# Optimization experiments

Hardware: AMD Instinct MI355X
Metric: run time of the kernel (lower is better)

The kernel has to match this reference:

```python
import jax, jax.numpy as jnp
import numpy as np

B = 2
SP = (480, 360, 32)   # spatial_shape (z, y, x)
GS = (8, 8, 8)        # query_gs_ratio
EP = (40, 15, 16)     # embed_params (pool compress ratio)
H = 8
N = 120000
D = 256
OUT = 20


def _dims(rat):
    return tuple((s + r - 1) // r for s, r in zip(SP, rat))


def sine_pe(coords, d_pos):
    # coords: [M,3] float voxel coords in original grid units; normalized sine PE
    nf = d_pos // 6
    sp = jnp.asarray(SP, jnp.float32)
    cn = coords / sp * (2.0 * jnp.pi)                      # normalize=True
    t = 10000.0 ** (jnp.arange(nf, dtype=jnp.float32) / nf)
    ang = cn[:, :, None] / t                               # [M,3,nf]
    pe = jnp.concatenate([jnp.sin(ang), jnp.cos(ang)], -1).reshape(coords.shape[0], -1)
    return jnp.pad(pe, ((0, 0), (0, d_pos - 6 * nf)))


def setup_inputs() -> dict:
    key = jax.random.key(0)
    ks = jax.random.split(key, 24)
    idx_b = jax.random.randint(ks[0], (N, 1), 0, B)
    idx_z = jax.random.randint(ks[1], (N, 1), 0, SP[0])
    idx_y = jax.random.randint(ks[2], (N, 1), 0, SP[1])
    idx_x = jax.random.randint(ks[3], (N, 1), 0, SP[2])
    indices = jnp.concatenate([idx_b, idx_z, idx_y, idx_x], axis=1).astype(jnp.int32)
    s = D ** -0.5
    p = lambda k, sh: jax.random.normal(k, sh, jnp.float32) * s
    return {
        'features': jax.random.normal(ks[4], (N, D), jnp.float32),
        'W_pool': p(ks[5], (D, D)), 'b_pool': jnp.zeros((D,), jnp.float32),
        'W_emb': p(ks[6], (D, D)), 'b_emb': jnp.zeros((D,), jnp.float32),
        'Wq': p(ks[7], (D, D)), 'bq': jnp.zeros((D,), jnp.float32),
        'Wk': p(ks[8], (D, D)), 'bk': jnp.zeros((D,), jnp.float32),
        'Wv': p(ks[9], (D, D)), 'bv': jnp.zeros((D,), jnp.float32),
        'Wo': p(ks[10], (D, D)), 'bo': jnp.zeros((D,), jnp.float32),
        'ln_g': jnp.ones((D,), jnp.float32), 'ln_b': jnp.zeros((D,), jnp.float32),
        'W_seg': p(ks[11], (D, OUT)), 'b_seg': jnp.zeros((OUT,), jnp.float32),
        'indices': indices,
        'batch_size': B,
    }


def reference(features, W_pool, b_pool, W_emb, b_emb, Wq, bq, Wk, bk, Wv, bv,
              Wo, bo, ln_g, ln_b, W_seg, b_seg, indices, batch_size):
    Zd, Yd, Xd = _dims(GS)
    Gq = Zd * Yd * Xd
    Sq = batch_size * Gq
    Ze, Ye, Xe = _dims(EP)
    Gk = Ze * Ye * Xe
    Sk = batch_size * Gk
    n = features.shape[0]

    # --- query pool branch: linear -> voxel-grid scatter_max ---
    pf = features @ W_pool + b_pool                                    # [N,D]
    dq = indices[:, 1:] // jnp.asarray(GS, jnp.int32)
    seg_q = ((indices[:, 0] * Zd + dq[:, 0]) * Yd + dq[:, 1]) * Xd + dq[:, 2]
    pool_max = jax.ops.segment_max(pf, seg_q, num_segments=Sq)
    cnt_q = jax.ops.segment_sum(jnp.ones((n,), jnp.float32), seg_q, num_segments=Sq)
    mq = cnt_q > 0
    pool_max = jnp.where(mq[:, None], pool_max, 0.0)
    cell = jnp.arange(Sq)
    rem = cell % Gq
    pool_c = jnp.stack([(rem // (Yd * Xd)) * GS[0],
                        ((rem // Xd) % Yd) * GS[1],
                        (rem % Xd) * GS[2]], -1).astype(jnp.float32)   # [Sq,3]

    # --- embedding branch ('pool'): linear -> coarse scatter_max + per-channel argmax coords ---
    ef = features @ W_emb + b_emb                                      # [N,D]
    de = indices[:, 1:] // jnp.asarray(EP, jnp.int32)
    seg_k = ((indices[:, 0] * Ze + de[:, 0]) * Ye + de[:, 1]) * Xe + de[:, 2]
    emb_max = jax.ops.segment_max(ef, seg_k, num_segments=Sk)
    cnt_k = jax.ops.segment_sum(jnp.ones((n,), jnp.float32), seg_k, num_segments=Sk)
    mk = cnt_k > 0
    emb_max = jnp.where(mk[:, None], emb_max, 0.0)
    winner = ef == jnp.where(mk[:, None], emb_max, -jnp.inf)[seg_k]
    idx = jax.ops.segment_max(jnp.where(winner, jnp.arange(n)[:, None], -1), seg_k, num_segments=Sk)
    idx_c = jnp.clip(idx, 0, n - 1)                                    # [Sk,D]
    ec = de.astype(jnp.float32)                                        # [N,3] downsampled coords
    emb_c = ec[idx_c].mean(axis=1) * jnp.asarray(EP, jnp.float32)      # [Sk,3]

    # --- position encoding (pointwise sine PE; per-batch loop in torch is pointwise-equivalent) ---
    pool_max = pool_max + sine_pe(pool_c, D)
    emb_max = emb_max + sine_pe(emb_c, D)

    # --- multi-head cross-attention (Q=pool, K/V=embedding), per-batch via dense grid reshape ---
    q_in = pool_max.reshape(batch_size, Gq, D)
    kv_in = emb_max.reshape(batch_size, Gk, D)
    dh = D // H
    q = (q_in @ Wq + bq).reshape(batch_size, Gq, H, dh)
    k = (kv_in @ Wk + bk).reshape(batch_size, Gk, H, dh)
    v = (kv_in @ Wv + bv).reshape(batch_size, Gk, H, dh)
    scores = jnp.einsum('bqhd,bkhd->bhqk', q, k) / jnp.float32(dh) ** 0.5
    kmask = mk.reshape(batch_size, Gk)
    scores = jnp.where(kmask[:, None, None, :], scores, -1e9)
    attn = jax.nn.softmax(scores, axis=-1)
    o = jnp.einsum('bhqk,bkhd->bqhd', attn, v).reshape(batch_size, Gq, D) @ Wo + bo
    h = q_in + o                                                       # residual + LayerNorm sublayer
    mu = h.mean(-1, keepdims=True)
    var = h.var(-1, keepdims=True)
    h = (h - mu) * jax.lax.rsqrt(var + 1e-5) * ln_g + ln_b
    feats_mhca = h.reshape(Sq, D)

    # --- gather back to voxels via pool_inv, residual, seg head (center-tap of SubMConv3d) ---
    vox = features + feats_mhca[seg_q]
    logits = vox @ W_seg + b_seg
    return logits
```

## Files before the change

kernel.cpp:

```cpp
#include <hip/hip_runtime.h>
#include <math.h>

#define N_PTS 120000
#define D 256
#define BATCH 2
#define NH 8
#define DH 32
#define OUTC 20

#define Zd 60
#define Yd 45
#define Xd 4
#define Gq 10800
#define Sq 21600

#define Ze 12
#define Ye 24
#define Xe 2
#define Gk 576
#define Sk 1152

typedef __bf16 bf16_t;
typedef __attribute__((ext_vector_type(8))) __bf16 bf16x8;
typedef __attribute__((ext_vector_type(4))) __bf16 bf16x4;
typedef __attribute__((ext_vector_type(4))) float f32x4;

__global__ __launch_bounds__(256) void k_prep(
    const float* __restrict__ Wp, const float* __restrict__ We,
    const float* __restrict__ Wq, const float* __restrict__ Wk,
    const float* __restrict__ Wv, const float* __restrict__ Wo,
    const float* __restrict__ bp, const float* __restrict__ be,
    const float* __restrict__ bk, const float* __restrict__ bv,
    bf16_t* __restrict__ Wpe, bf16_t* __restrict__ Wqt,
    bf16_t* __restrict__ Wkv, bf16_t* __restrict__ Wot,
    float* __restrict__ bpe, float* __restrict__ bkv)
{
    int n = blockIdx.x, k = threadIdx.x;
    if (n < 512) {
        const float* S = (n < 256) ? Wp : We;
        int nn = n & 255;
        Wpe[n * 256 + k] = (bf16_t)S[k * 256 + nn];
    } else if (n < 768) {
        int nn = n - 512;
        Wqt[nn * 256 + k] = (bf16_t)Wq[k * 256 + nn];
    } else if (n < 1280) {
        int m2 = n - 768;
        const float* S = (m2 < 256) ? Wk : Wv;
        int nn = m2 & 255;
        Wkv[m2 * 256 + k] = (bf16_t)S[k * 256 + nn];
    } else if (n < 1536) {
        int nn = n - 1280;
        Wot[nn * 256 + k] = (bf16_t)Wo[k * 256 + nn];
    } else {
        bpe[k] = bp[k]; bpe[256 + k] = be[k];
        bkv[k] = bk[k]; bkv[256 + k] = bv[k];
    }
}

__global__ __launch_bounds__(256) void k_count(
    const int* __restrict__ indices, int* __restrict__ cnt_q, int* __restrict__ cnt_k,
    int* __restrict__ segq, int* __restrict__ segk)
{
    int i = blockIdx.x * 256 + threadIdx.x;
    if (i >= N_PTS) return;
    const int* id = indices + (size_t)i * 4;
    int b = id[0], z = id[1], y = id[2], x = id[3];
    int sq = ((b * Zd + (z >> 3)) * Yd + (y >> 3)) * Xd + (x >> 3);
    int sk = ((b * Ze + (z / 40)) * Ye + (y / 15)) * Xe + (x >> 4);
    segq[i] = sq; segk[i] = sk;
    atomicAdd(&cnt_q[sq], 1);
    atomicAdd(&cnt_k[sk], 1);
}

__global__ __launch_bounds__(1024) void k_scan(
    const int* __restrict__ cnt, int n, int* __restrict__ offs, int* __restrict__ cursor)
{
    __shared__ int wbase[17];
    __shared__ int carry_s;
    const int t = threadIdx.x, lane = t & 63, w = t >> 6;
    if (t == 0) carry_s = 0;
    __syncthreads();
    for (int base = 0; base < n; base += 1024) {
        int v = (base + t < n) ? cnt[base + t] : 0;
        int incl = v;
        #pragma unroll
        for (int off = 1; off < 64; off <<= 1) {
            int u = __shfl_up(incl, off);
            if (lane >= off) incl += u;
        }
        if (lane == 63) wbase[w + 1] = incl;
        __syncthreads();
        if (t == 0) {
            int s = 0;
            wbase[0] = 0;
            #pragma unroll
            for (int i = 1; i <= 16; ++i) { s += wbase[i]; wbase[i] = s; }
        }
        __syncthreads();
        int excl = incl - v + wbase[w] + carry_s;
        if (base + t < n) { offs[base + t] = excl; cursor[base + t] = excl; }
        __syncthreads();
        if (t == 0) carry_s += wbase[16];
        __syncthreads();
    }
}

__global__ __launch_bounds__(256) void k_place(
    const int* __restrict__ segq, const int* __restrict__ segk,
    int* __restrict__ cur_q, int* __restrict__ cur_k,
    int* __restrict__ ids_q, int* __restrict__ ids_k)
{
    int i = blockIdx.x * 256 + threadIdx.x;
    if (i >= N_PTS) return;
    ids_q[atomicAdd(&cur_q[segq[i]], 1)] = i;
    ids_k[atomicAdd(&cur_k[segk[i]], 1)] = i;
}

__global__ __launch_bounds__(512, 2) void k_gemm(
    const float* __restrict__ A, int M,
    const bf16_t* __restrict__ Wt, const float* __restrict__ bias,
    int mode, float* __restrict__ outp, int ldo)
{
    __shared__ __align__(16) bf16_t Abuf[128][72];
    __shared__ __align__(16) bf16_t Bbuf[256][72];

    const int t = threadIdx.x;
    const int wave = t >> 6, lane = t & 63;
    const int wr = wave >> 2, wc = wave & 3;
    const int lrow = lane & 15, quad = lane >> 4;
    const int row0 = blockIdx.y * 128;
    const int ntile = blockIdx.x;

    f32x4 acc[4][4];
    #pragma unroll
    for (int mi = 0; mi < 4; ++mi)
        #pragma unroll
        for (int ni = 0; ni < 4; ++ni)
            acc[mi][ni] = (f32x4){0.f, 0.f, 0.f, 0.f};

    for (int k0 = 0; k0 < 256; k0 += 64) {
        #pragma unroll
        for (int i = 0; i < 4; ++i) {
            int c = i * 512 + t;
            int r = c >> 4, c4 = c & 15;
            float4 v = make_float4(0.f, 0.f, 0.f, 0.f);
            if (row0 + r < M)
                v = *(const float4*)(A + (size_t)(row0 + r) * 256 + k0 + c4 * 4);
            bf16x4 bv4;
            bv4[0] = (bf16_t)v.x; bv4[1] = (bf16_t)v.y;
            bv4[2] = (bf16_t)v.z; bv4[3] = (bf16_t)v.w;
            *(bf16x4*)&Abuf[r][c4 * 4] = bv4;
        }
        #pragma unroll
        for (int i = 0; i < 4; ++i) {
            int c = i * 512 + t;
            int r = c >> 3, c8 = c & 7;
            uint4 w = *(const uint4*)(Wt + ((size_t)(ntile * 256 + r)) * 256 + k0 + c8 * 8);
            *(uint4*)&Bbuf[r][c8 * 8] = w;
        }
        __syncthreads();

        #pragma unroll
        for (int kk = 0; kk < 64; kk += 32) {
            bf16x8 Af[4], Bf[4];
            #pragma unroll
            for (int mi = 0; mi < 4; ++mi)
                Af[mi] = *(const bf16x8*)&Abuf[wr * 64 + mi * 16 + lrow][kk + quad * 8];
            #pragma unroll
            for (int ni = 0; ni < 4; ++ni)
                Bf[ni] = *(const bf16x8*)&Bbuf[wc * 64 + ni * 16 + lrow][kk + quad * 8];
            #pragma unroll
            for (int mi = 0; mi < 4; ++mi)
                #pragma unroll
                for (int ni = 0; ni < 4; ++ni)
                    acc[mi][ni] = __builtin_amdgcn_mfma_f32_16x16x32_bf16(
                        Af[mi], Bf[ni], acc[mi][ni], 0, 0, 0);
        }
        __syncthreads();
    }

    const int colb = ntile * 256 + wc * 64;
    float biasv[4];
    #pragma unroll
    for (int ni = 0; ni < 4; ++ni) biasv[ni] = bias[colb + ni * 16 + lrow];

    if (mode == 0) {
        #pragma unroll
        for (int mi = 0; mi < 4; ++mi) {
            int lr = wr * 64 + mi * 16 + quad * 4;
            #pragma unroll
            for (int reg = 0; reg < 4; ++reg) {
                int grow = row0 + lr + reg;
                if (grow >= M) continue;
                #pragma unroll
                for (int ni = 0; ni < 4; ++ni) {
                    int col = colb + ni * 16 + lrow;
                    outp[(size_t)grow * ldo + col] = acc[mi][ni][reg] + biasv[ni];
                }
            }
        }
    } else {
        bf16_t* outb = (bf16_t*)outp;
        #pragma unroll
        for (int mi = 0; mi < 4; ++mi) {
            int lr = wr * 64 + mi * 16 + quad * 4;
            #pragma unroll
            for (int reg = 0; reg < 4; ++reg) {
                int grow = row0 + lr + reg;
                if (grow >= M) continue;
                #pragma unroll
                for (int ni = 0; ni < 4; ++ni) {
                    int col = colb + ni * 16 + lrow;
                    outb[(size_t)grow * ldo + col] = (bf16_t)(acc[mi][ni][reg] + biasv[ni]);
                }
            }
        }
    }
}

__device__ inline float pe_val(int j, float cz, float cy, float cx) {
    if (j >= 252) return 0.f;
    int dim = j / 84;
    int f = j % 84;
    int fi = (f >= 42) ? (f - 42) : f;
    float c  = (dim == 0) ? cz : ((dim == 1) ? cy : cx);
    float sp = (dim == 0) ? 480.f : ((dim == 1) ? 360.f : 32.f);
    float cn = c / sp * 6.28318530717958647692f;
    float tt = expf((float)fi * (9.210340371976184f / 42.f));
    float ang = cn / tt;
    return (f >= 42) ? cosf(ang) : sinf(ang);
}

__global__ __launch_bounds__(256) void k_pool_q(
    const bf16_t* __restrict__ pfb, const int* __restrict__ ids,
    const int* __restrict__ offs, const int* __restrict__ cnt,
    float* __restrict__ out)
{
    const int t = threadIdx.x, lane = t & 63, w = t >> 6;
    const int s = blockIdx.x * 4 + w;
    if (s >= Sq) return;
    const int count = cnt[s], start = offs[s];
    float mx[4] = {-3.0e38f, -3.0e38f, -3.0e38f, -3.0e38f};
    for (int r = 0; r < count; ++r) {
        int i = ids[start + r];
        bf16x4 v = *(const bf16x4*)(pfb + (size_t)i * 256 + lane * 4);
        #pragma unroll
        for (int j = 0; j < 4; ++j) mx[j] = fmaxf(mx[j], (float)v[j]);
    }
    int rem = s % Gq;
    float cz = (float)((rem / (Yd * Xd)) * 8);
    float cy = (float)(((rem / Xd) % Yd) * 8);
    float cx = (float)((rem % Xd) * 8);
    #pragma unroll
    for (int j = 0; j < 4; ++j) {
        float v = (count > 0) ? mx[j] : 0.f;
        out[(size_t)s * 256 + lane * 4 + j] = v + pe_val(lane * 4 + j, cz, cy, cx);
    }
}

__global__ __launch_bounds__(512) void k_pool_k(
    const bf16_t* __restrict__ efb, const int* __restrict__ ids,
    const int* __restrict__ offs, const int* __restrict__ cnt,
    float* __restrict__ out, int* __restrict__ kmask)
{
    __shared__ float red[8][256];
    const int t = threadIdx.x, lane = t & 63, w = t >> 6;
    const int s = blockIdx.x;
    const int count = cnt[s], start = offs[s];
    float mx[4] = {-3.0e38f, -3.0e38f, -3.0e38f, -3.0e38f};
    for (int r = w; r < count; r += 8) {
        int i = ids[start + r];
        bf16x4 v = *(const bf16x4*)(efb + (size_t)i * 256 + lane * 4);
        #pragma unroll
        for (int j = 0; j < 4; ++j) mx[j] = fmaxf(mx[j], (float)v[j]);
    }
    #pragma unroll
    for (int j = 0; j < 4; ++j) red[w][lane * 4 + j] = mx[j];
    __syncthreads();
    if (t < 256) {
        float m = red[0][t];
        #pragma unroll
        for (int i = 1; i < 8; ++i) m = fmaxf(m, red[i][t]);
        if (count == 0) m = 0.f;
        int rem = s % Gk;
        float cz = (float)((rem / (Ye * Xe)) * 40);
        float cy = (float)(((rem / Xe) % Ye) * 15);
        float cx = (float)((rem % Xe) * 16);
        out[(size_t)s * 256 + t] = m + pe_val(t, cz, cy, cx);
        if (t == 0) kmask[s] = (count > 0) ? 1 : 0;
    }
}

__global__ __launch_bounds__(256) void k_attn_mfma(
    const bf16_t* __restrict__ Q, const bf16_t* __restrict__ KV,
    const int* __restrict__ kmask, float* __restrict__ O)
{
    __shared__ __align__(16) bf16_t Qs[64][40];
    __shared__ __align__(16) bf16_t Ks[192][40];
    __shared__ __align__(16) bf16_t Vts[32][200];
    __shared__ __align__(16) bf16_t Ps[4][16][200];
    __shared__ float mskf[192];

    const int bh = blockIdx.y;
    const int b = bh >> 3, h = bh & 7;
    const int t = threadIdx.x, wave = t >> 6, lane = t & 63;
    const int lrow = lane & 15, quad = lane >> 4;
    const int q0 = blockIdx.x * 64;

    {
        int r = t >> 2, part = t & 3;
        int qi = q0 + r;
        uint4 val = make_uint4(0u, 0u, 0u, 0u);
        if (qi < Gq)
            val = *(const uint4*)(Q + ((size_t)(b * Gq + qi)) * 256 + h * 32 + part * 8);
        *(uint4*)&Qs[r][part * 8] = val;
    }
    __syncthreads();

    const bf16x8 Aq = *(const bf16x8*)&Qs[wave * 16 + lrow][quad * 8];

    f32x4 oacc[2];
    oacc[0] = (f32x4){0.f, 0.f, 0.f, 0.f};
    oacc[1] = (f32x4){0.f, 0.f, 0.f, 0.f};
    float m_run[4], l_run[4];
    #pragma unroll
    for (int r = 0; r < 4; ++r) { m_run[r] = -3.0e38f; l_run[r] = 0.f; }

    for (int c0 = 0; c0 < Gk; c0 += 192) {
        __syncthreads();
        #pragma unroll
        for (int i = 0; i < 3; ++i) {
            int idx = i * 256 + t;
            int kk = idx >> 2, part = idx & 3;
            uint4 val = *(const uint4*)(KV + ((size_t)(b * Gk + c0 + kk)) * 512 + h * 32 + part * 8);
            *(uint4*)&Ks[kk][part * 8] = val;
        }
        #pragma unroll
        for (int i = 0; i < 3; ++i) {
            int idx = i * 256 + t;
            int kk = idx >> 2, part = idx & 3;
            bf16x8 v = *(const bf16x8*)(KV + ((size_t)(b * Gk + c0 + kk)) * 512 + 256 + h * 32 + part * 8);
            #pragma unroll
            for (int j = 0; j < 8; ++j)
                Vts[part * 8 + j][kk] = v[j];
        }
        if (t < 192) mskf[t] = kmask[b * Gk + c0 + t] ? 0.f : -1.0e9f;
        __syncthreads();

        float sreg[12][4];
        #pragma unroll
        for (int nt = 0; nt < 12; ++nt) {
            bf16x8 Bk = *(const bf16x8*)&Ks[nt * 16 + lrow][quad * 8];
            f32x4 sacc = __builtin_amdgcn_mfma_f32_16x16x32_bf16(
                Aq, Bk, (f32x4){0.f, 0.f, 0.f, 0.f}, 0, 0, 0);
            float pen = mskf[nt * 16 + lrow];
            #pragma unroll
            for (int r = 0; r < 4; ++r)
                sreg[nt][r] = sacc[r] * 0.17677669529663688f + pen;
        }

        float alpha[4];
        #pragma unroll
        for (int r = 0; r < 4; ++r) {
            float mx = sreg[0][r];
            #pragma unroll
            for (int nt = 1; nt < 12; ++nt) mx = fmaxf(mx, sreg[nt][r]);
            #pragma unroll
            for (int off = 1; off < 16; off <<= 1)
                mx = fmaxf(mx, __shfl_xor(mx, off));
            float mnew = fmaxf(m_run[r], mx);
            alpha[r] = __expf(m_run[r] - mnew);
            m_run[r] = mnew;
            l_run[r] *= alpha[r];
        }
        #pragma unroll
        for (int n2 = 0; n2 < 2; ++n2)
            #pragma unroll
            for (int r = 0; r < 4; ++r) oacc[n2][r] *= alpha[r];

        float psum[4] = {0.f, 0.f, 0.f, 0.f};
        #pragma unroll
        for (int nt = 0; nt < 12; ++nt) {
            #pragma unroll
            for (int r = 0; r < 4; ++r) {
                float p = __expf(sreg[nt][r] - m_run[r]);
                psum[r] += p;
                Ps[wave][quad * 4 + r][nt * 16 + lrow] = (bf16_t)p;
            }
        }
        #pragma unroll
        for (int r = 0; r < 4; ++r) {
            float s = psum[r];
            #pragma unroll
            for (int off = 1; off < 16; off <<= 1) s += __shfl_xor(s, off);
            l_run[r] += s;
        }

        #pragma unroll
        for (int ks = 0; ks < 6; ++ks) {
            bf16x8 Ap = *(const bf16x8*)&Ps[wave][lrow][ks * 32 + quad * 8];
            #pragma unroll
            for (int n2 = 0; n2 < 2; ++n2) {
                bf16x8 Bv = *(const bf16x8*)&Vts[n2 * 16 + lrow][ks * 32 + quad * 8];
                oacc[n2] = __builtin_amdgcn_mfma_f32_16x16x32_bf16(
                    Ap, Bv, oacc[n2], 0, 0, 0);
            }
        }
    }

    #pragma unroll
    for (int r = 0; r < 4; ++r) {
        int qi = q0 + wave * 16 + quad * 4 + r;
        if (qi >= Gq) continue;
        float inv = (l_run[r] > 0.f) ? (1.f / l_run[r]) : 0.f;
        #pragma unroll
        for (int n2 = 0; n2 < 2; ++n2)
            O[((size_t)(b * Gq + qi)) * 256 + h * 32 + n2 * 16 + lrow] = oacc[n2][r] * inv;
    }
}

__global__ __launch_bounds__(256) void k_ln(
    const float* __restrict__ oproj, const float* __restrict__ resid,
    const float* __restrict__ g, const float* __restrict__ bta,
    float* __restrict__ out)
{
    const int s = blockIdx.x, t = threadIdx.x;
    float h = resid[(size_t)s * D + t] + oproj[(size_t)s * D + t];

    float s1 = h, s2 = h * h;
    for (int o = 32; o > 0; o >>= 1) {
        s1 += __shfl_down(s1, o);
        s2 += __shfl_down(s2, o);
    }
    __shared__ float r1[4], r2[4];
    __shared__ float mu_s, rstd_s;
    int w = t >> 6;
    if ((t & 63) == 0) { r1[w] = s1; r2[w] = s2; }
    __syncthreads();
    if (t == 0) {
        float a = r1[0] + r1[1] + r1[2] + r1[3];
        float bsum = r2[0] + r2[1] + r2[2] + r2[3];
        float mu = a * (1.f / 256.f);
        float var = bsum * (1.f / 256.f) - mu * mu;
        mu_s = mu;
        rstd_s = rsqrtf(var + 1e-5f);
    }
    __syncthreads();
    out[(size_t)s * D + t] = (h - mu_s) * rstd_s * g[t] + bta[t];
}

#define PTS 16
__global__ __launch_bounds__(320) void k_logits(
    const float* __restrict__ feat, const float* __restrict__ mhca,
    const int* __restrict__ indices, const float* __restrict__ Wseg,
    const float* __restrict__ bseg, float* __restrict__ out)
{
    __shared__ float vox[PTS][D + 1];
    __shared__ float Wl[D * OUTC];
    __shared__ int sq[PTS];
    const int t = threadIdx.x;
    const int p0 = blockIdx.x * PTS;

    if (t < PTS) {
        const int* id = indices + (size_t)(p0 + t) * 4;
        sq[t] = ((id[0] * Zd + (id[1] >> 3)) * Yd + (id[2] >> 3)) * Xd + (id[3] >> 3);
    }
    for (int idx = t; idx < D * OUTC; idx += 320) Wl[idx] = Wseg[idx];
    __syncthreads();
    for (int idx = t; idx < PTS * D; idx += 320) {
        int r = idx / D, k = idx % D;
        vox[r][k] = feat[(size_t)(p0 + r) * D + k] + mhca[(size_t)sq[r] * D + k];
    }
    __syncthreads();

    const int r = t / OUTC, o = t % OUTC;
    float acc = bseg[o];
    #pragma unroll 4
    for (int k = 0; k < D; ++k) acc += vox[r][k] * Wl[k * OUTC + o];
    out[(size_t)(p0 + r) * OUTC + o] = acc;
}

extern "C" void kernel_launch(void* const* d_in, const int* in_sizes, int n_in,
                              void* d_out, int out_size, void* d_ws, size_t ws_size,
                              hipStream_t stream) {
    const float* features = (const float*)d_in[0];
    const float* W_pool = (const float*)d_in[1];
    const float* b_pool = (const float*)d_in[2];
    const float* W_emb  = (const float*)d_in[3];
    const float* b_emb  = (const float*)d_in[4];
    const float* Wq = (const float*)d_in[5];
    const float* bq = (const float*)d_in[6];
    const float* Wk = (const float*)d_in[7];
    const float* bk = (const float*)d_in[8];
    const float* Wv = (const float*)d_in[9];
    const float* bv = (const float*)d_in[10];
    const float* Wo = (const float*)d_in[11];
    const float* bo = (const float*)d_in[12];
    const float* ln_g = (const float*)d_in[13];
    const float* ln_b = (const float*)d_in[14];
    const float* W_seg = (const float*)d_in[15];
    const float* b_seg = (const float*)d_in[16];
    const int* indices = (const int*)d_in[17];
    float* out = (float*)d_out;

    float* ws = (float*)d_ws;
    const size_t SQD = (size_t)Sq * D;
    const size_t SKD = (size_t)Sk * D;
    const size_t PFB_FL = (size_t)N_PTS * D / 2;

    size_t oP   = 0;
    size_t oPF  = oP + PFB_FL;
    size_t oEF  = oPF + SQD;
    size_t oWpe = oEF + SKD;
    size_t oWqt = oWpe + 65536;
    size_t oWkv = oWqt + 32768;
    size_t oWot = oWkv + 65536;
    size_t obpe = oWot + 32768;
    size_t obkv = obpe + 512;
    size_t oCnt = obkv + 512;
    size_t oOffq = oCnt + 21600 + 1152;
    size_t oCurq = oOffq + 21600;
    size_t oOffk = oCurq + 21600;
    size_t oCurk = oOffk + 1152;
    size_t oSegq = oCurk + 1152;
    size_t oSegk = oSegq + N_PTS;
    size_t oIdsq = oSegk + N_PTS;
    size_t oIdsk = oIdsq + N_PTS;
    size_t oKm   = oIdsk + N_PTS;

    bf16_t* pfb = (bf16_t*)(ws + oP);
    float* pool_feat = ws + oPF;
    float* emb_feat  = ws + oEF;
    bf16_t* Wpe = (bf16_t*)(ws + oWpe);
    bf16_t* Wqt = (bf16_t*)(ws + oWqt);
    bf16_t* Wkv = (bf16_t*)(ws + oWkv);
    bf16_t* Wot = (bf16_t*)(ws + oWot);
    float* bpe = ws + obpe;
    float* bkv = ws + obkv;
    int* cnt_q = (int*)(ws + oCnt);
    int* cnt_k = cnt_q + 21600;
    int* offs_q = (int*)(ws + oOffq);
    int* cur_q  = (int*)(ws + oCurq);
    int* offs_k = (int*)(ws + oOffk);
    int* cur_k  = (int*)(ws + oCurk);
    int* segq = (int*)(ws + oSegq);
    int* segk = (int*)(ws + oSegk);
    int* ids_q = (int*)(ws + oIdsq);
    int* ids_k = (int*)(ws + oIdsk);
    int* kmask = (int*)(ws + oKm);

    bf16_t* Qb  = (bf16_t*)(ws + oP);
    bf16_t* KVb = (bf16_t*)(ws + oP + 2764800);
    float* attnO = ws + oP + 3059712;
    float* oproj = ws + oP + 8589312;
    float* mhca  = ws + oP + 3059712;

    hipMemsetAsync(cnt_q, 0, (21600 + 1152) * sizeof(int), stream);

    k_prep<<<1537, 256, 0, stream>>>(W_pool, W_emb, Wq, Wk, Wv, Wo,
                                     b_pool, b_emb, bk, bv,
                                     Wpe, Wqt, Wkv, Wot, bpe, bkv);

    k_count<<<(N_PTS + 255) / 256, 256, 0, stream>>>(indices, cnt_q, cnt_k, segq, segk);
    k_scan<<<1, 1024, 0, stream>>>(cnt_q, 21600, offs_q, cur_q);
    k_scan<<<1, 1024, 0, stream>>>(cnt_k, 1152, offs_k, cur_k);
    k_place<<<(N_PTS + 255) / 256, 256, 0, stream>>>(segq, segk, cur_q, cur_k, ids_q, ids_k);

    {
        dim3 g(1, (N_PTS + 127) / 128);
        k_gemm<<<g, 512, 0, stream>>>(features, N_PTS, Wpe + 256 * 256, bpe + 256, 2,
                                      (float*)pfb, 256);
    }
    k_pool_k<<<Sk, 512, 0, stream>>>(pfb, ids_k, offs_k, cnt_k, emb_feat, kmask);

    {
        dim3 g(1, (N_PTS + 127) / 128);
        k_gemm<<<g, 512, 0, stream>>>(features, N_PTS, Wpe, bpe, 2,
                                      (float*)pfb, 256);
    }
    k_pool_q<<<(Sq + 3) / 4, 256, 0, stream>>>(pfb, ids_q, offs_q, cnt_q, pool_feat);

    {
        dim3 g(1, (Sq + 127) / 128);
        k_gemm<<<g, 512, 0, stream>>>(pool_feat, Sq, Wqt, bq, 2, (float*)Qb, 256);
    }
    {
        dim3 g(2, (Sk + 127) / 128);
        k_gemm<<<g, 512, 0, stream>>>(emb_feat, Sk, Wkv, bkv, 2, (float*)KVb, 512);
    }

    {
        dim3 ag((Gq + 63) / 64, BATCH * NH);
        k_attn_mfma<<<ag, 256, 0, stream>>>(Qb, KVb, kmask, attnO);
    }

    {
        dim3 g(1, (Sq + 127) / 128);
        k_gemm<<<g, 512, 0, stream>>>(attnO, Sq, Wot, bo, 0, oproj, 256);
    }

    k_ln<<<Sq, 256, 0, stream>>>(oproj, pool_feat, ln_g, ln_b, mhca);

    k_logits<<<N_PTS / PTS, 320, 0, stream>>>(
        features, mhca, indices, W_seg, b_seg, out);
}
```

Measured before the change: 708.9 us.

## Rewrite segmentation head logits as bf16 MFMA GEMM with padded weights

Replaces the scalar FMA logits kernel, which processed 16 points per block and reloaded the full seg weight into LDS each time, with a 128-row-tile bf16 MFMA kernel. The W_seg weights are transposed and zero-padded to 32 outputs in the prep kernel. The voxel plus mhca sum is converted to bf16 in LDS before the matrix multiply. This aims to cut per-block weight reload and scalar compute cost, at the price of bf16 rounding on the final projection and wasted work on the padded output columns.

```diff
diff --git a/kernel.cpp b/kernel.cpp
--- a/kernel.cpp
+++ b/kernel.cpp
@@ -31,9 +31,12 @@
     const float* __restrict__ Wv, const float* __restrict__ Wo,
     const float* __restrict__ bp, const float* __restrict__ be,
     const float* __restrict__ bk, const float* __restrict__ bv,
+    const float* __restrict__ Wseg, const float* __restrict__ bseg,
     bf16_t* __restrict__ Wpe, bf16_t* __restrict__ Wqt,
     bf16_t* __restrict__ Wkv, bf16_t* __restrict__ Wot,
-    float* __restrict__ bpe, float* __restrict__ bkv)
+    bf16_t* __restrict__ Wsegt,
+    float* __restrict__ bpe, float* __restrict__ bkv,
+    float* __restrict__ bsegp)
 {
     int n = blockIdx.x, k = threadIdx.x;
     if (n < 512) {
@@ -51,9 +54,13 @@
     } else if (n < 1536) {
         int nn = n - 1280;
         Wot[nn * 256 + k] = (bf16_t)Wo[k * 256 + nn];
-    } else {
+    } else if (n == 1536) {
         bpe[k] = bp[k]; bpe[256 + k] = be[k];
         bkv[k] = bk[k]; bkv[256 + k] = bv[k];
+        if (k < 32) bsegp[k] = (k < OUTC) ? bseg[k] : 0.f;
+    } else {
+        int n2 = n - 1537;
+        Wsegt[n2 * 256 + k] = (n2 < OUTC) ? (bf16_t)Wseg[k * OUTC + n2] : (bf16_t)0.f;
     }
 }
 
@@ -449,35 +456,82 @@
     out[(size_t)s * D + t] = (h - mu_s) * rstd_s * g[t] + bta[t];
 }
 
-#define PTS 16
-__global__ __launch_bounds__(320) void k_logits(
+__global__ __launch_bounds__(512, 2) void k_logits_mfma(
     const float* __restrict__ feat, const float* __restrict__ mhca,
-    const int* __restrict__ indices, const float* __restrict__ Wseg,
-    const float* __restrict__ bseg, float* __restrict__ out)
-{
-    __shared__ float vox[PTS][D + 1];
-    __shared__ float Wl[D * OUTC];
-    __shared__ int sq[PTS];
+    const int* __restrict__ indices, const bf16_t* __restrict__ Wsegt,
+    const float* __restrict__ bsegp, float* __restrict__ out)
+{
+    __shared__ __align__(16) bf16_t Abuf[128][72];
+    __shared__ __align__(16) bf16_t Bbuf[32][72];
+    __shared__ int sq_s[128];
+
     const int t = threadIdx.x;
-    const int p0 = blockIdx.x * PTS;
-
-    if (t < PTS) {
-        const int* id = indices + (size_t)(p0 + t) * 4;
-        sq[t] = ((id[0] * Zd + (id[1] >> 3)) * Yd + (id[2] >> 3)) * Xd + (id[3] >> 3);
-    }
-    for (int idx = t; idx < D * OUTC; idx += 320) Wl[idx] = Wseg[idx];
+    const int wave = t >> 6, lane = t & 63;
+    const int lrow = lane & 15, quad = lane >> 4;
+    const int row0 = blockIdx.x * 128;
+
+    if (t < 128) {
+        int row = row0 + t;
+        if (row < N_PTS) {
+            const int* id = indices + (size_t)row * 4;
+            sq_s[t] = ((id[0] * Zd + (id[1] >> 3)) * Yd + (id[2] >> 3)) * Xd + (id[3] >> 3);
+        } else sq_s[t] = 0;
+    }
     __syncthreads();
-    for (int idx = t; idx < PTS * D; idx += 320) {
-        int r = idx / D, k = idx % D;
-        vox[r][k] = feat[(size_t)(p0 + r) * D + k] + mhca[(size_t)sq[r] * D + k];
-    }
-    __syncthreads();
-
-    const int r = t / OUTC, o = t % OUTC;
-    float acc = bseg[o];
-    #pragma unroll 4
-    for (int k = 0; k < D; ++k) acc += vox[r][k] * Wl[k * OUTC + o];
-    out[(size_t)(p0 + r) * OUTC + o] = acc;
+
+    f32x4 acc[2];
+    acc[0] = (f32x4){0.f, 0.f, 0.f, 0.f};
+    acc[1] = (f32x4){0.f, 0.f, 0.f, 0.f};
+
+    for (int k0 = 0; k0 < 256; k0 += 64) {
+        #pragma unroll
+        for (int i = 0; i < 4; ++i) {
+            int c = i * 512 + t;
+            int r = c >> 4, c4 = c & 15;
+            float4 v = make_float4(0.f, 0.f, 0.f, 0.f);
+            int grow = row0 + r;
+            if (grow < N_PTS) {
+                v = *(const float4*)(feat + (size_t)grow * 256 + k0 + c4 * 4);
+                float4 m = *(const float4*)(mhca + (size_t)sq_s[r] * 256 + k0 + c4 * 4);
+                v.x += m.x; v.y += m.y; v.z += m.z; v.w += m.w;
+            }
+            bf16x4 bv4;
+            bv4[0] = (bf16_t)v.x; bv4[1] = (bf16_t)v.y;
+            bv4[2] = (bf16_t)v.z; bv4[3] = (bf16_t)v.w;
+            *(bf16x4*)&Abuf[r][c4 * 4] = bv4;
+        }
+        if (t < 256) {
+            int r = t >> 3, c8 = t & 7;
+            uint4 w = *(const uint4*)(Wsegt + (size_t)r * 256 + k0 + c8 * 8);
+            *(uint4*)&Bbuf[r][c8 * 8] = w;
+        }
+        __syncthreads();
+
+        #pragma unroll
+        for (int kk = 0; kk < 64; kk += 32) {
+            bf16x8 Af = *(const bf16x8*)&Abuf[wave * 16 + lrow][kk + quad * 8];
+            #pragma unroll
+            for (int ni = 0; ni < 2; ++ni) {
+                bf16x8 Bf = *(const bf16x8*)&Bbuf[ni * 16 + lrow][kk + quad * 8];
+                acc[ni] = __builtin_amdgcn_mfma_f32_16x16x32_bf16(
+                    Af, Bf, acc[ni], 0, 0, 0);
+            }
+        }
+        __syncthreads();
+    }
+
+    #pragma unroll
+    for (int ni = 0; ni < 2; ++ni) {
+        int col = ni * 16 + lrow;
+        if (col >= OUTC) continue;
+        float bias = bsegp[col];
+        #pragma unroll
+        for (int reg = 0; reg < 4; ++reg) {
+            int grow = row0 + wave * 16 + quad * 4 + reg;
+            if (grow >= N_PTS) continue;
+            out[(size_t)grow * OUTC + col] = acc[ni][reg] + bias;
+        }
+    }
 }
 
 extern "C" void kernel_launch(void* const* d_in, const int* in_sizes, int n_in,
@@ -527,6 +581,8 @@
     size_t oIdsq = oSegk + N_PTS;
     size_t oIdsk = oIdsq + N_PTS;
     size_t oKm   = oIdsk + N_PTS;
+    size_t oWst  = oKm + 1152;
+    size_t obsg  = oWst + 4096;
 
     bf16_t* pfb = (bf16_t*)(ws + oP);
     float* pool_feat = ws + oPF;
@@ -548,6 +604,8 @@
     int* ids_q = (int*)(ws + oIdsq);
     int* ids_k = (int*)(ws + oIdsk);
     int* kmask = (int*)(ws + oKm);
+    bf16_t* Wsegt = (bf16_t*)(ws + oWst);
+    float* bsegp = ws + obsg;
 
     bf16_t* Qb  = (bf16_t*)(ws + oP);
     bf16_t* KVb = (bf16_t*)(ws + oP + 2764800);
@@ -557,9 +615,9 @@
 
     hipMemsetAsync(cnt_q, 0, (21600 + 1152) * sizeof(int), stream);
 
-    k_prep<<<1537, 256, 0, stream>>>(W_pool, W_emb, Wq, Wk, Wv, Wo,
-                                     b_pool, b_emb, bk, bv,
-                                     Wpe, Wqt, Wkv, Wot, bpe, bkv);
+    k_prep<<<1569, 256, 0, stream>>>(W_pool, W_emb, Wq, Wk, Wv, Wo,
+                                     b_pool, b_emb, bk, bv, W_seg, b_seg,
+                                     Wpe, Wqt, Wkv, Wot, Wsegt, bpe, bkv, bsegp);
 
     k_count<<<(N_PTS + 255) / 256, 256, 0, stream>>>(indices, cnt_q, cnt_k, segq, segk);
     k_scan<<<1, 1024, 0, stream>>>(cnt_q, 21600, offs_q, cur_q);
@@ -601,6 +659,6 @@
 
     k_ln<<<Sq, 256, 0, stream>>>(oproj, pool_feat, ln_g, ln_b, mhca);
 
-    k_logits<<<N_PTS / PTS, 320, 0, stream>>>(
-        features, mhca, indices, W_seg, b_seg, out);
-}
+    k_logits_mfma<<<(N_PTS + 127) / 128, 512, 0, stream>>>(
+        features, mhca, indices, Wsegt, bsegp, out);
+}
```

Measured after the change: 603.4 us. 14.9% less time.
